# Kernel optimization log

Hardware: AMD Instinct MI355X
Metric: run time of the kernel (lower is better)

The kernel has to match this reference:

```python
import jax, jax.numpy as jnp
import numpy as np

IN_FEATURES = 4096
OUT_FEATURES = 16384

def setup_inputs() -> dict:
    key = jax.random.key(0)
    k1, k2 = jax.random.split(key)
    x = jax.random.normal(k1, (4, 2048, IN_FEATURES), dtype=jnp.float32)
    # init_weights: uniform(-1, 1)
    W = jax.random.uniform(k2, (OUT_FEATURES, IN_FEATURES), dtype=jnp.float32, minval=-1.0, maxval=1.0)
    b = jnp.zeros((OUT_FEATURES,), dtype=jnp.float32)
    return {"x": x, "W": W, "b": b}

def reference(x, W, b):
    # Binarize weights to {-1, 0, +1} via sign, then dense linear: y = x @ sign(W)^T + b
    Wb = jnp.sign(W)
    return jnp.einsum('bsd,od->bso', x, Wb) + b
```

## Files before the change

kernel.cpp:

```cpp
#include <hip/hip_runtime.h>
#include <hip/hip_bf16.h>

#define M_TOT 8192
#define N_TOT 16384
#define K_TOT 4096
#define NT (K_TOT / 64)

typedef int i32x4 __attribute__((ext_vector_type(4)));
typedef int i32x16 __attribute__((ext_vector_type(16)));
typedef __bf16 bf16x8 __attribute__((ext_vector_type(8)));
typedef float f32x4 __attribute__((ext_vector_type(4)));

#define GLOAD_LDS16(g, l)                                                     \
  __builtin_amdgcn_global_load_lds(                                           \
      (__attribute__((address_space(1))) const void*)(g),                     \
      (__attribute__((address_space(3))) void*)(l), 16, 0, 0)

__device__ __forceinline__ ushort f2bf_rne(float f) {
  unsigned u = __float_as_uint(f);
  u += 0x7FFFu + ((u >> 16) & 1u);
  return (ushort)(u >> 16);
}
__device__ __forceinline__ ushort sgn_bf16(float w) {
  return w > 0.f ? (ushort)0x3F80u : (w < 0.f ? (ushort)0xBF80u : (ushort)0u);
}


__global__ void quant_x_kernel(const float* __restrict__ x,
                               char* __restrict__ At, float* __restrict__ s) {
  int row = blockIdx.x;
  int tid = threadIdx.x;
  const float4* xr = (const float4*)(x + (size_t)row * K_TOT + tid * 16);
  float4 v[4];
  float amax = 0.f;
#pragma unroll
  for (int j = 0; j < 4; ++j) {
    v[j] = xr[j];
    amax = fmaxf(amax, fmaxf(fmaxf(fabsf(v[j].x), fabsf(v[j].y)),
                             fmaxf(fabsf(v[j].z), fabsf(v[j].w))));
  }
#pragma unroll
  for (int o = 32; o > 0; o >>= 1) amax = fmaxf(amax, __shfl_xor(amax, o));
  __shared__ float wmax[4];
  if ((tid & 63) == 0) wmax[tid >> 6] = amax;
  __syncthreads();
  amax = fmaxf(fmaxf(wmax[0], wmax[1]), fmaxf(wmax[2], wmax[3]));
  float inv = amax > 0.f ? 127.0f / amax : 0.f;
  if (tid == 0) s[row] = amax * (1.0f / 127.0f);
  int q[16];
#pragma unroll
  for (int j = 0; j < 4; ++j) {
    q[j * 4 + 0] = max(-127, min(127, __float2int_rn(v[j].x * inv)));
    q[j * 4 + 1] = max(-127, min(127, __float2int_rn(v[j].y * inv)));
    q[j * 4 + 2] = max(-127, min(127, __float2int_rn(v[j].z * inv)));
    q[j * 4 + 3] = max(-127, min(127, __float2int_rn(v[j].w * inv)));
  }
  int4 o4;
  int* op = (int*)&o4;
#pragma unroll
  for (int j = 0; j < 4; ++j)
    op[j] = (q[j * 4] & 255) | ((q[j * 4 + 1] & 255) << 8) |
            ((q[j * 4 + 2] & 255) << 16) | ((q[j * 4 + 3] & 255) << 24);
  int r32 = row >> 5, l31 = row & 31;
  int kt = tid >> 2, ks = (tid >> 1) & 1, hi = tid & 1;
  size_t dst = ((size_t)(r32 * 128 + kt * 2 + ks) << 10) + ((hi * 32 + l31) << 4);
  *(int4*)(At + dst) = o4;
}

__global__ void quant_w_kernel(const float* __restrict__ w,
                               char* __restrict__ Bt) {
  int n32 = blockIdx.x;
  int t = threadIdx.x;
#pragma unroll 4
  for (int i = 0; i < 32; ++i) {
    int c = i * 256 + t;
    int kt = c >> 7, ks = (c >> 6) & 1, l = c & 63;
    int n = n32 * 32 + (l & 31);
    int k = kt * 64 + ks * 32 + (l >> 5) * 16;
    const float4* src = (const float4*)(w + (size_t)n * K_TOT + k);
    int4 o4;
    int* op = (int*)&o4;
#pragma unroll
    for (int j = 0; j < 4; ++j) {
      float4 v = src[j];
      int q0 = v.x > 0.f ? 1 : (v.x < 0.f ? -1 : 0);
      int q1 = v.y > 0.f ? 1 : (v.y < 0.f ? -1 : 0);
      int q2 = v.z > 0.f ? 1 : (v.z < 0.f ? -1 : 0);
      int q3 = v.w > 0.f ? 1 : (v.w < 0.f ? -1 : 0);
      op[j] = (q0 & 255) | ((q1 & 255) << 8) | ((q2 & 255) << 16) |
              ((q3 & 255) << 24);
    }
    *(int4*)(Bt + ((size_t)n32 << 17) + ((size_t)c << 4)) = o4;
  }
}

__global__ __launch_bounds__(512, 2) void gemm_i8_pipe(
    const char* __restrict__ At, const char* __restrict__ Bt,
    const float* __restrict__ s, const float* __restrict__ bias,
    float* __restrict__ C) {
  __shared__ char lds[4][32768];

  int bid = blockIdx.x;
  int wg = (bid & 7) * 256 + (bid >> 3);
  int bnS = wg >> 8;
  int rem = wg & 255;
  int bm = rem >> 3;
  int bn = bnS * 8 + (rem & 7);
  int rowBase = bm * 256;
  int colBase = bn * 256;

  int t = threadIdx.x;
  int lane = t & 63;
  int wave = t >> 6;
  int wr = wave >> 2;
  int wc = wave & 3;
  int l31 = lane & 31;
  int hi = lane >> 5;

  const char* gAp[2];
  const char* gBp[2];
#pragma unroll
  for (int q = 0; q < 2; ++q) {
    int ss = t + 512 * q;
    int g = ss >> 6;
    int r32l = g >> 1, ks = g & 1;
    int j = ss & 63;
    gAp[q] = At + ((size_t)((bm * 8 + r32l) * 128 + ks) << 10) + (j << 4);
    gBp[q] = Bt + ((size_t)((bn * 8 + r32l) * 128 + ks) << 10) + (j << 4);
  }

  i32x16 acc[4][2] = {};
  i32x4 Xa[4], Xb[2], Ya[4], Yb[2];

#define STAGE(kt_, buf_)                                                      \
  {                                                                           \
    size_t _o = (size_t)(kt_) << 11;                                          \
    GLOAD_LDS16(gAp[0] + _o, &lds[buf_][t * 16]);                             \
    GLOAD_LDS16(gAp[1] + _o, &lds[buf_][8192 + t * 16]);                      \
    GLOAD_LDS16(gBp[0] + _o, &lds[buf_][16384 + t * 16]);                     \
    GLOAD_LDS16(gBp[1] + _o, &lds[buf_][24576 + t * 16]);                     \
  }
#define READF(Adst, Bdst, buf_, ks_)                                          \
  {                                                                           \
    const char* _la = &lds[buf_][0];                                          \
    const char* _lb = _la + 16384;                                            \
    _Pragma("unroll") for (int mi = 0; mi < 4; ++mi)                          \
        Adst[mi] = *(const i32x4*)(_la + (((wr * 4 + mi) * 2 + (ks_)) << 10) + \
                                   (lane << 4));                              \
    _Pragma("unroll") for (int ni = 0; ni < 2; ++ni)                          \
        Bdst[ni] = *(const i32x4*)(_lb + (((wc * 2 + ni) * 2 + (ks_)) << 10) + \
                                   (lane << 4));                              \
  }
#define MFMACL(Asrc, Bsrc)                                                    \
  {                                                                           \
    __builtin_amdgcn_s_setprio(1);                                            \
    _Pragma("unroll") for (int mi = 0; mi < 4; ++mi) {                        \
      acc[mi][0] = __builtin_amdgcn_mfma_i32_32x32x32_i8(Asrc[mi], Bsrc[0],   \
                                                         acc[mi][0], 0, 0, 0); \
      acc[mi][1] = __builtin_amdgcn_mfma_i32_32x32x32_i8(Asrc[mi], Bsrc[1],   \
                                                         acc[mi][1], 0, 0, 0); \
    }                                                                         \
    __builtin_amdgcn_s_setprio(0);                                            \
  }

  STAGE(0, 0);
  STAGE(1, 1);
  asm volatile("s_waitcnt vmcnt(4)" ::: "memory");
  __builtin_amdgcn_sched_barrier(0);
  __builtin_amdgcn_s_barrier();
  __builtin_amdgcn_sched_barrier(0);
  READF(Xa, Xb, 0, 0);

  for (int tt = 0; tt < NT; ++tt) {
    int buf = tt & 3;
    if (tt + 2 < NT) STAGE(tt + 2, (tt + 2) & 3);
    READF(Ya, Yb, buf, 1);
    MFMACL(Xa, Xb);
    if (tt + 2 < NT) {
      asm volatile("s_waitcnt vmcnt(4)" ::: "memory");
    } else if (tt + 1 < NT) {
      asm volatile("s_waitcnt vmcnt(0)" ::: "memory");
    }
    __builtin_amdgcn_sched_barrier(0);
    __builtin_amdgcn_s_barrier();
    __builtin_amdgcn_sched_barrier(0);
    if (tt + 1 < NT) READF(Xa, Xb, (tt + 1) & 3, 0);
    MFMACL(Ya, Yb);
  }

#undef MFMACL
#undef READF
#undef STAGE

#pragma unroll
  for (int mi = 0; mi < 4; ++mi) {
#pragma unroll
    for (int ni = 0; ni < 2; ++ni) {
      int gc = colBase + wc * 64 + ni * 32 + l31;
      float bv = bias[gc];
#pragma unroll
      for (int rg = 0; rg < 16; ++rg) {
        int rowIn = (rg & 3) + 8 * (rg >> 2) + 4 * hi;
        int gr = rowBase + wr * 128 + mi * 32 + rowIn;
        C[(size_t)gr * N_TOT + gc] = (float)acc[mi][ni][rg] * s[gr] + bv;
      }
    }
  }
}

__global__ void gemm_fused_kernel(const float* __restrict__ A,
                                  const float* __restrict__ W,
                                  const float* __restrict__ bias,
                                  float* __restrict__ C) {
  __shared__ ushort lsA[128 * 32];
  __shared__ ushort lsB[128 * 32];

  int nwg = gridDim.x;
  int bid = blockIdx.x;
  int wg = (bid & 7) * (nwg >> 3) + (bid >> 3);
  const int NBN = N_TOT / 128;
  int bm = wg / NBN;
  int bn = wg % NBN;
  int rowBase = bm * 128;
  int colBase = bn * 128;

  int t = threadIdx.x;
  int lane = t & 63;
  int wave = t >> 6;
  int wm = (wave >> 1) * 64;
  int wn = (wave & 1) * 64;

  f32x4 acc[4][4] = {};

  int srow = t >> 3;
  int scol = (t & 7) * 4;
  int fr = lane & 15;
  int koff = (lane >> 4) * 8;

  for (int k0 = 0; k0 < K_TOT; k0 += 32) {
    float4 va[4], vb[4];
#pragma unroll
    for (int r = 0; r < 4; ++r) {
      va[r] = *(const float4*)&A[(size_t)(rowBase + r * 32 + srow) * K_TOT + k0 + scol];
      vb[r] = *(const float4*)&W[(size_t)(colBase + r * 32 + srow) * K_TOT + k0 + scol];
    }
    __syncthreads();
#pragma unroll
    for (int r = 0; r < 4; ++r) {
      int e = r * 1024 + t * 4;
      ushort4 oa, ob;
      oa.x = f2bf_rne(va[r].x); oa.y = f2bf_rne(va[r].y);
      oa.z = f2bf_rne(va[r].z); oa.w = f2bf_rne(va[r].w);
      ob.x = sgn_bf16(vb[r].x); ob.y = sgn_bf16(vb[r].y);
      ob.z = sgn_bf16(vb[r].z); ob.w = sgn_bf16(vb[r].w);
      *(ushort4*)&lsA[e] = oa;
      *(ushort4*)&lsB[e] = ob;
    }
    __syncthreads();

    bf16x8 af[4], bfr[4];
#pragma unroll
    for (int i = 0; i < 4; ++i)
      af[i] = *(const bf16x8*)&lsA[(wm + i * 16 + fr) * 32 + koff];
#pragma unroll
    for (int j = 0; j < 4; ++j)
      bfr[j] = *(const bf16x8*)&lsB[(wn + j * 16 + fr) * 32 + koff];

#pragma unroll
    for (int i = 0; i < 4; ++i)
#pragma unroll
      for (int j = 0; j < 4; ++j)
        acc[i][j] = __builtin_amdgcn_mfma_f32_16x16x32_bf16(af[i], bfr[j],
                                                            acc[i][j], 0, 0, 0);
  }

  int orow0 = rowBase + wm + ((lane >> 4) << 2);
  int ocol0 = colBase + wn + (lane & 15);
#pragma unroll
  for (int i = 0; i < 4; ++i) {
#pragma unroll
    for (int j = 0; j < 4; ++j) {
      int col = ocol0 + j * 16;
      float bv = bias[col];
#pragma unroll
      for (int rg = 0; rg < 4; ++rg) {
        int row = orow0 + i * 16 + rg;
        C[(size_t)row * N_TOT + col] = acc[i][j][rg] + bv;
      }
    }
  }
}

extern "C" void kernel_launch(void* const* d_in, const int* in_sizes, int n_in,
                              void* d_out, int out_size, void* d_ws,
                              size_t ws_size, hipStream_t stream) {
  const float* x = (const float*)d_in[0];
  const float* W = (const float*)d_in[1];
  const float* b = (const float*)d_in[2];
  float* out = (float*)d_out;

  const size_t xq_bytes = (size_t)M_TOT * K_TOT;
  const size_t wq_bytes = (size_t)N_TOT * K_TOT;
  const size_t need = xq_bytes + wq_bytes + M_TOT * 4;

  if (ws_size >= need) {
    char* At = (char*)d_ws;
    char* Bt = At + xq_bytes;
    float* s = (float*)(Bt + wq_bytes);
    quant_x_kernel<<<M_TOT, 256, 0, stream>>>(x, At, s);
    quant_w_kernel<<<N_TOT / 32, 256, 0, stream>>>(W, Bt);
    const int nblocks = (M_TOT / 256) * (N_TOT / 256);
    gemm_i8_pipe<<<nblocks, 512, 0, stream>>>(At, Bt, s, b, out);
  } else {
    const int nblocks = (M_TOT / 128) * (N_TOT / 128);
    gemm_fused_kernel<<<nblocks, 256, 0, stream>>>(x, W, b, out);
  }
}
```

Before: 664.9 us.

## Widen int8 GEMM K-tile to 128 with a double-buffered LDS pipeline

Doubles the K depth of each staged LDS tile from 64 to 128. The pipeline changes from four 32KB buffers prefetched two tiles ahead to two 64KB buffers prefetched one tile ahead. Each iteration now runs four MFMA groups between one load wait and one barrier, so there are half as many block-wide synchronisations. In exchange, the full vmcnt(0) drain each iteration gives a shallower prefetch pipeline, which may expose more global-load latency.

```diff
diff --git a/kernel.cpp b/kernel.cpp
--- a/kernel.cpp
+++ b/kernel.cpp
@@ -4,7 +4,7 @@
 #define M_TOT 8192
 #define N_TOT 16384
 #define K_TOT 4096
-#define NT (K_TOT / 64)
+#define NT2 (K_TOT / 128)
 
 typedef int i32x4 __attribute__((ext_vector_type(4)));
 typedef int i32x16 __attribute__((ext_vector_type(16)));
@@ -94,11 +94,11 @@
   }
 }
 
-__global__ __launch_bounds__(512, 2) void gemm_i8_pipe(
+__global__ __launch_bounds__(512, 2) void gemm_i8_bk128(
     const char* __restrict__ At, const char* __restrict__ Bt,
     const float* __restrict__ s, const float* __restrict__ bias,
     float* __restrict__ C) {
-  __shared__ char lds[4][32768];
+  __shared__ char lds[2][65536];
 
   int bid = blockIdx.x;
   int wg = (bid & 7) * 256 + (bid >> 3);
@@ -117,38 +117,42 @@
   int l31 = lane & 31;
   int hi = lane >> 5;
 
-  const char* gAp[2];
-  const char* gBp[2];
-#pragma unroll
-  for (int q = 0; q < 2; ++q) {
+  const char* gAp[4];
+  const char* gBp[4];
+#pragma unroll
+  for (int q = 0; q < 4; ++q) {
     int ss = t + 512 * q;
     int g = ss >> 6;
-    int r32l = g >> 1, ks = g & 1;
+    int r32l = g >> 2, kk = g & 3;
     int j = ss & 63;
-    gAp[q] = At + ((size_t)((bm * 8 + r32l) * 128 + ks) << 10) + (j << 4);
-    gBp[q] = Bt + ((size_t)((bn * 8 + r32l) * 128 + ks) << 10) + (j << 4);
+    gAp[q] = At + ((size_t)((bm * 8 + r32l) * 128 + kk) << 10) + (j << 4);
+    gBp[q] = Bt + ((size_t)((bn * 8 + r32l) * 128 + kk) << 10) + (j << 4);
   }
 
   i32x16 acc[4][2] = {};
   i32x4 Xa[4], Xb[2], Ya[4], Yb[2];
 
-#define STAGE(kt_, buf_)                                                      \
+#define STAGE(T_, buf_)                                                       \
   {                                                                           \
-    size_t _o = (size_t)(kt_) << 11;                                          \
+    size_t _o = (size_t)(T_) << 12;                                           \
     GLOAD_LDS16(gAp[0] + _o, &lds[buf_][t * 16]);                             \
     GLOAD_LDS16(gAp[1] + _o, &lds[buf_][8192 + t * 16]);                      \
-    GLOAD_LDS16(gBp[0] + _o, &lds[buf_][16384 + t * 16]);                     \
-    GLOAD_LDS16(gBp[1] + _o, &lds[buf_][24576 + t * 16]);                     \
-  }
-#define READF(Adst, Bdst, buf_, ks_)                                          \
+    GLOAD_LDS16(gAp[2] + _o, &lds[buf_][16384 + t * 16]);                     \
+    GLOAD_LDS16(gAp[3] + _o, &lds[buf_][24576 + t * 16]);                     \
+    GLOAD_LDS16(gBp[0] + _o, &lds[buf_][32768 + t * 16]);                     \
+    GLOAD_LDS16(gBp[1] + _o, &lds[buf_][40960 + t * 16]);                     \
+    GLOAD_LDS16(gBp[2] + _o, &lds[buf_][49152 + t * 16]);                     \
+    GLOAD_LDS16(gBp[3] + _o, &lds[buf_][57344 + t * 16]);                     \
+  }
+#define READF(Adst, Bdst, buf_, kq_)                                          \
   {                                                                           \
     const char* _la = &lds[buf_][0];                                          \
-    const char* _lb = _la + 16384;                                            \
+    const char* _lb = _la + 32768;                                            \
     _Pragma("unroll") for (int mi = 0; mi < 4; ++mi)                          \
-        Adst[mi] = *(const i32x4*)(_la + (((wr * 4 + mi) * 2 + (ks_)) << 10) + \
+        Adst[mi] = *(const i32x4*)(_la + (((wr * 4 + mi) * 4 + (kq_)) << 10) + \
                                    (lane << 4));                              \
     _Pragma("unroll") for (int ni = 0; ni < 2; ++ni)                          \
-        Bdst[ni] = *(const i32x4*)(_lb + (((wc * 2 + ni) * 2 + (ks_)) << 10) + \
+        Bdst[ni] = *(const i32x4*)(_lb + (((wc * 2 + ni) * 4 + (kq_)) << 10) + \
                                    (lane << 4));                              \
   }
 #define MFMACL(Asrc, Bsrc)                                                    \
@@ -164,28 +168,29 @@
   }
 
   STAGE(0, 0);
-  STAGE(1, 1);
-  asm volatile("s_waitcnt vmcnt(4)" ::: "memory");
+  asm volatile("s_waitcnt vmcnt(0)" ::: "memory");
   __builtin_amdgcn_sched_barrier(0);
   __builtin_amdgcn_s_barrier();
   __builtin_amdgcn_sched_barrier(0);
   READF(Xa, Xb, 0, 0);
 
-  for (int tt = 0; tt < NT; ++tt) {
-    int buf = tt & 3;
-    if (tt + 2 < NT) STAGE(tt + 2, (tt + 2) & 3);
-    READF(Ya, Yb, buf, 1);
+  for (int tt = 0; tt < NT2; ++tt) {
+    int b = tt & 1;
+    if (tt + 1 < NT2) STAGE(tt + 1, b ^ 1);
+    READF(Ya, Yb, b, 1);
     MFMACL(Xa, Xb);
-    if (tt + 2 < NT) {
-      asm volatile("s_waitcnt vmcnt(4)" ::: "memory");
-    } else if (tt + 1 < NT) {
+    READF(Xa, Xb, b, 2);
+    MFMACL(Ya, Yb);
+    READF(Ya, Yb, b, 3);
+    MFMACL(Xa, Xb);
+    MFMACL(Ya, Yb);
+    if (tt + 1 < NT2) {
       asm volatile("s_waitcnt vmcnt(0)" ::: "memory");
-    }
-    __builtin_amdgcn_sched_barrier(0);
-    __builtin_amdgcn_s_barrier();
-    __builtin_amdgcn_sched_barrier(0);
-    if (tt + 1 < NT) READF(Xa, Xb, (tt + 1) & 3, 0);
-    MFMACL(Ya, Yb);
+      __builtin_amdgcn_sched_barrier(0);
+      __builtin_amdgcn_s_barrier();
+      __builtin_amdgcn_sched_barrier(0);
+      READF(Xa, Xb, b ^ 1, 0);
+    }
   }
 
 #undef MFMACL
@@ -310,7 +315,7 @@
     quant_x_kernel<<<M_TOT, 256, 0, stream>>>(x, At, s);
     quant_w_kernel<<<N_TOT / 32, 256, 0, stream>>>(W, Bt);
     const int nblocks = (M_TOT / 256) * (N_TOT / 256);
-    gemm_i8_pipe<<<nblocks, 512, 0, stream>>>(At, Bt, s, b, out);
+    gemm_i8_bk128<<<nblocks, 512, 0, stream>>>(At, Bt, s, b, out);
   } else {
     const int nblocks = (M_TOT / 128) * (N_TOT / 128);
     gemm_fused_kernel<<<nblocks, 256, 0, stream>>>(x, W, b, out);
```

Result: slower. 682.0 us (+2.6%).
